# Kernel tuning notes

Measured on AMD Instinct MI355X. Metric: run time of the kernel, lower is better.

Reference implementation:

```python
import jax, jax.numpy as jnp
import numpy as np

K = 2          # downsample rate
H = 8          # attention heads
D_LLM = 1024
DK = D_LLM // H
N_LAYER = 2
F_HID = D_LLM // 4  # 256, per PositionwiseFeedForward(llm_dim, llm_dim//4)
EPS = 1e-12


def _ln(x, g, b):
    m = jnp.mean(x, axis=-1, keepdims=True)
    v = jnp.mean((x - m) ** 2, axis=-1, keepdims=True)
    return (x - m) * jax.lax.rsqrt(v + EPS) * g + b


def setup_inputs() -> dict:
    key = jax.random.key(0)
    ks = jax.random.split(key, 16)
    s = 0.02
    d_in = 512 * K   # encoder_dim * k = 1024
    d_ff = 2048
    inp = {
        'x':  jax.random.normal(ks[0], (8, 2048, 512), dtype=jnp.float32),
        'W1': jax.random.normal(ks[1], (d_ff, d_in)) * s,
        'b1': jnp.zeros((d_ff,)),
        'W2': jax.random.normal(ks[2], (D_LLM, d_ff)) * s,
        'b2': jnp.zeros((D_LLM,)),
        'ln1_g': jnp.ones((N_LAYER, D_LLM)), 'ln1_b': jnp.zeros((N_LAYER, D_LLM)),
        'ln2_g': jnp.ones((N_LAYER, D_LLM)), 'ln2_b': jnp.zeros((N_LAYER, D_LLM)),
        'Wq': jax.random.normal(ks[3], (N_LAYER, D_LLM, D_LLM)) * s, 'bq': jnp.zeros((N_LAYER, D_LLM)),
        'Wk': jax.random.normal(ks[4], (N_LAYER, D_LLM, D_LLM)) * s, 'bk': jnp.zeros((N_LAYER, D_LLM)),
        'Wv': jax.random.normal(ks[5], (N_LAYER, D_LLM, D_LLM)) * s, 'bv': jnp.zeros((N_LAYER, D_LLM)),
        'Wo': jax.random.normal(ks[6], (N_LAYER, D_LLM, D_LLM)) * s, 'bo': jnp.zeros((N_LAYER, D_LLM)),
        'Fw1': jax.random.normal(ks[7], (N_LAYER, F_HID, D_LLM)) * s, 'Fb1': jnp.zeros((N_LAYER, F_HID)),
        'Fw2': jax.random.normal(ks[8], (N_LAYER, D_LLM, F_HID)) * s, 'Fb2': jnp.zeros((N_LAYER, D_LLM)),
    }
    return inp


def reference(x, W1, b1, W2, b2, ln1_g, ln1_b, ln2_g, ln2_b,
              Wq, bq, Wk, bk, Wv, bv, Wo, bo, Fw1, Fb1, Fw2, Fb2):
    B, S, D = x.shape
    chunk = (S - 1) // K + 1
    pad = chunk * K - S
    x = jnp.pad(x, ((0, 0), (0, pad), (0, 0)))
    x = x.reshape(B, chunk, K * D)                    # [B, T, k*D]
    # downsample projection: linear2(relu(linear1(x)))
    x = jax.nn.relu(x @ W1.T + b1) @ W2.T + b2        # [B, T, D_LLM]
    T = chunk
    for l in range(N_LAYER):
        # --- self-attention sublayer (pre-norm) ---
        resid = x
        h = _ln(x, ln1_g[l], ln1_b[l])
        q = (h @ Wq[l].T + bq[l]).reshape(B, T, H, DK).transpose(0, 2, 1, 3)
        k_ = (h @ Wk[l].T + bk[l]).reshape(B, T, H, DK).transpose(0, 2, 1, 3)
        v = (h @ Wv[l].T + bv[l]).reshape(B, T, H, DK).transpose(0, 2, 1, 3)
        scores = jnp.einsum('bhqd,bhkd->bhqk', q, k_) * (DK ** -0.5)
        attn = jax.nn.softmax(scores, axis=-1)        # mask is None
        o = jnp.einsum('bhqk,bhkd->bhqd', attn, v)
        o = o.transpose(0, 2, 1, 3).reshape(B, T, H * DK)
        x = resid + o @ Wo[l].T + bo[l]
        # --- FFN sublayer (pre-norm) ---
        resid = x
        h = _ln(x, ln2_g[l], ln2_b[l])
        x = resid + jax.nn.relu(h @ Fw1[l].T + Fb1[l]) @ Fw2[l].T + Fb2[l]
    return x
```

## Files before the change

kernel.cpp:

```cpp
#include <hip/hip_runtime.h>
#include <hip/hip_bf16.h>


#define DMODEL 1024
#define DFF 2048
#define FHID 256
#define NHEAD 8
#define DKH 128
#define TSEQ 1024

typedef __hip_bfloat16 bf16;
typedef __attribute__((ext_vector_type(8))) short bf16x8;
typedef __attribute__((ext_vector_type(4))) float f32x4;

#define MFMA16(a, b, c) __builtin_amdgcn_mfma_f32_16x16x32_bf16(a, b, c, 0, 0, 0)

__device__ int g_is_bf16;

__device__ __forceinline__ bool flagbf_block() {
    __shared__ int fsh;
    if (threadIdx.x == 0)
        fsh = __hip_atomic_load(&g_is_bf16, __ATOMIC_ACQUIRE,
                                __HIP_MEMORY_SCOPE_AGENT);
    __syncthreads();
    return fsh != 0;
}
__device__ __forceinline__ float gload(const void* p, size_t i, bool bf) {
    return bf ? __bfloat162float(((const bf16*)p)[i]) : ((const float*)p)[i];
}
__device__ __forceinline__ void gstore(void* p, size_t i, bool bf, float v) {
    if (bf) ((bf16*)p)[i] = __float2bfloat16(v);
    else    ((float*)p)[i] = v;
}

__device__ __forceinline__ void async16(const bf16* g, const bf16* l) {
    __builtin_amdgcn_global_load_lds(
        (const __attribute__((address_space(1))) void*)g,
        (__attribute__((address_space(3))) void*)l, 16, 0, 0);
}

__global__ void detect_kernel(const void* __restrict__ probe) {
    const int lane = threadIdx.x & 63;
    const bf16* h = (const bf16*)probe;
    int ok = 1;
    #pragma unroll
    for (int j = 0; j < 4; ++j) {
        float v = __bfloat162float(h[lane * 4 + j]);
        if (!(fabsf(v) <= 1000.0f)) ok = 0;
    }
    unsigned long long m = __ballot(ok);
    if (lane == 0)
        __hip_atomic_store(&g_is_bf16, m == ~0ull ? 1 : 0, __ATOMIC_RELEASE,
                           __HIP_MEMORY_SCOPE_AGENT);
}

#define O_W1  0ull
#define O_W2  2097152ull
#define O_QK  4194304ull
#define O_WV  8388608ull
#define O_WO  10485760ull
#define O_F1  12582912ull
#define O_F2  13107200ull
#define ARENA_ELEMS 13631488ull

__global__ __launch_bounds__(256) void cvt_weights(
        const void* W1, const void* W2, const void* Wq, const void* Wk,
        const void* Wv, const void* Wo, const void* F1, const void* F2,
        bf16* __restrict__ arena) {
    if (flagbf_block()) return;
    int b = blockIdx.x;
    const float* src; bf16* dst;
    if      (b < 128)  {           src = (const float*)W1 + (size_t)b * 16384;
                         dst = arena + O_W1 + (size_t)b * 16384; }
    else if (b < 256)  { b -= 128; src = (const float*)W2 + (size_t)b * 16384;
                         dst = arena + O_W2 + (size_t)b * 16384; }
    else if (b < 384)  { b -= 256; src = (const float*)Wq + (size_t)b * 16384;
                         dst = arena + O_QK + (size_t)(b >> 6) * 2097152
                                            + (size_t)(b & 63) * 16384; }
    else if (b < 512)  { b -= 384; src = (const float*)Wk + (size_t)b * 16384;
                         dst = arena + O_QK + (size_t)(b >> 6) * 2097152
                                            + 1048576 + (size_t)(b & 63) * 16384; }
    else if (b < 640)  { b -= 512; src = (const float*)Wv + (size_t)b * 16384;
                         dst = arena + O_WV + (size_t)b * 16384; }
    else if (b < 768)  { b -= 640; src = (const float*)Wo + (size_t)b * 16384;
                         dst = arena + O_WO + (size_t)b * 16384; }
    else if (b < 800)  { b -= 768; src = (const float*)F1 + (size_t)b * 16384;
                         dst = arena + O_F1 + (size_t)b * 16384; }
    else               { b -= 800; src = (const float*)F2 + (size_t)b * 16384;
                         dst = arena + O_F2 + (size_t)b * 16384; }
    const int tid = threadIdx.x;
    #pragma unroll
    for (int it = 0; it < 16; ++it) {
        const int e = it * 1024 + tid * 4;
        float4 f = *(const float4*)(src + e);
        bf16 t[4] = {__float2bfloat16(f.x), __float2bfloat16(f.y),
                     __float2bfloat16(f.z), __float2bfloat16(f.w)};
        *(uint2*)(dst + e) = *(const uint2*)t;
    }
}

__global__ __launch_bounds__(256) void cvt_x(
        const void* __restrict__ X, size_t x_off, bf16* __restrict__ dst) {
    if (flagbf_block()) return;
    const float* src = (const float*)X + x_off + (size_t)blockIdx.x * 16384;
    bf16* d = dst + (size_t)blockIdx.x * 16384;
    const int tid = threadIdx.x;
    #pragma unroll
    for (int it = 0; it < 16; ++it) {
        const int e = it * 1024 + tid * 4;
        float4 f = *(const float4*)(src + e);
        bf16 t[4] = {__float2bfloat16(f.x), __float2bfloat16(f.y),
                     __float2bfloat16(f.z), __float2bfloat16(f.w)};
        *(uint2*)(d + e) = *(const uint2*)t;
    }
}

template <bool RELU, bool ADD, int CMODE, bool TRANSC, bool BIAS2>
__global__ __launch_bounds__(512, 4) void gemm256(
        const bf16* Abf, const bf16* Acv,
        const bf16* Wlo_bf, const bf16* Whi_bf,
        const bf16* Wlo_cv, const bf16* Whi_cv,
        const void* __restrict__ bias, const void* __restrict__ bias2,
        size_t b_off,
        void* __restrict__ C, size_t c_off,
        int M, int N, int K) {
    const bool fl = flagbf_block();
    const bf16* A   = fl ? Abf : Acv;
    const bf16* Wlo = fl ? Wlo_bf : Wlo_cv;
    const bf16* Whi = fl ? Whi_bf : Whi_cv;

    __shared__ __align__(16) bf16 As[2][256 * 32];
    __shared__ __align__(16) bf16 Bs[2][128 * 32];

    const int gx = gridDim.x;
    const int lin = blockIdx.x + gx * blockIdx.y;
    int bm, bn;
    if ((gridDim.y & 7) == 0) {
        const int xcd = lin & 7, j = lin >> 3;
        const int rpx = gridDim.y >> 3;
        bm = (xcd * rpx + (j / gx)) * 256;
        bn = (j % gx) * 128;
    } else {
        bm = blockIdx.y * 256;
        bn = blockIdx.x * 128;
    }

    const int tid = threadIdx.x;
    const int wave = tid >> 6, lane = tid & 63;
    const int quad = lane >> 4, l15 = lane & 15;
    const int wm = wave >> 1, wn = wave & 1;

    const bf16* Wp;
    int bnr;
    if (BIAS2 && bn >= 1024) { Wp = Whi; bnr = bn - 1024; }
    else                     { Wp = Wlo; bnr = bn; }

    const int srow = lane >> 2;
    const int schunk = (lane & 3) ^ ((lane >> 3) & 3);
    const bf16* gaBase = A  + (size_t)(bm  + wave * 32 + srow) * K + schunk * 8;
    const bf16* gbBase = Wp + (size_t)(bnr + wave * 16 + srow) * K + schunk * 8;
    const int laOff0 = (wave * 32) * 32;
    const int laOff1 = (wave * 32 + 16) * 32;
    const int lbOff  = (wave * 16) * 32;

    f32x4 acc[4][4];
    #pragma unroll
    for (int i = 0; i < 4; ++i)
        #pragma unroll
        for (int j = 0; j < 4; ++j) acc[i][j] = (f32x4){0.f, 0.f, 0.f, 0.f};

    const int nt = K >> 5;
    int cur = 0;

    async16(gaBase, &As[0][laOff0]);
    async16(gaBase + (size_t)16 * K, &As[0][laOff1]);
    async16(gbBase, &Bs[0][lbOff]);
    __asm__ __volatile__("s_waitcnt vmcnt(0)" ::: "memory");
    __syncthreads();

    for (int t = 0; t < nt; ++t) {
        if (t + 1 < nt) {
            const int kn = (t + 1) << 5;
            async16(gaBase + kn, &As[cur ^ 1][laOff0]);
            async16(gaBase + (size_t)16 * K + kn, &As[cur ^ 1][laOff1]);
            async16(gbBase + kn, &Bs[cur ^ 1][lbOff]);
        }
        bf16x8 bfr[4];
        #pragma unroll
        for (int ni = 0; ni < 4; ++ni) {
            const int row = wn * 64 + ni * 16 + l15;
            bfr[ni] = *(const bf16x8*)
                &Bs[cur][row * 32 + ((quad ^ ((row >> 1) & 3)) << 3)];
        }
        #pragma unroll
        for (int mi = 0; mi < 4; ++mi) {
            const int row = wm * 64 + mi * 16 + l15;
            bf16x8 af = *(const bf16x8*)
                &As[cur][row * 32 + ((quad ^ ((row >> 1) & 3)) << 3)];
            #pragma unroll
            for (int ni = 0; ni < 4; ++ni)
                acc[mi][ni] = MFMA16(af, bfr[ni], acc[mi][ni]);
        }
        __syncthreads();
        cur ^= 1;
    }

    const bool cbf = CMODE ? fl : true;
    #pragma unroll
    for (int ni = 0; ni < 4; ++ni) {
        const int col = bn + wn * 64 + ni * 16 + l15;
        float bv;
        if (BIAS2) bv = col < 1024 ? gload(bias, b_off + col, fl)
                                   : gload(bias2, b_off + col - 1024, fl);
        else       bv = gload(bias, b_off + col, fl);
        #pragma unroll
        for (int mi = 0; mi < 4; ++mi) {
            const int row0 = bm + wm * 64 + mi * 16 + quad * 4;
            if (TRANSC) {
                bf16 pk[4];
                #pragma unroll
                for (int rr = 0; rr < 4; ++rr)
                    pk[rr] = __float2bfloat16(acc[mi][ni][rr] + bv);
                *(uint2*)((bf16*)C + c_off + (size_t)col * M + row0) =
                    *(const uint2*)pk;
            } else {
                #pragma unroll
                for (int rr = 0; rr < 4; ++rr) {
                    float v = acc[mi][ni][rr] + bv;
                    if (RELU) v = fmaxf(v, 0.f);
                    size_t idx = c_off + (size_t)(row0 + rr) * N + col;
                    if (ADD) v += gload(C, idx, cbf);
                    gstore(C, idx, cbf, v);
                }
            }
        }
    }
}

template <bool RELU, bool ADD, int CMODE, bool TRANSC, bool BIAS2>
__global__ __launch_bounds__(256) void gemm_bf16(
        const bf16* Abf, const bf16* Acv,
        const bf16* Wlo_bf, const bf16* Whi_bf,
        const bf16* Wlo_cv, const bf16* Whi_cv,
        const void* __restrict__ bias, const void* __restrict__ bias2,
        size_t b_off,
        void* __restrict__ C, size_t c_off,
        int M, int N, int K) {
    const bool fl = flagbf_block();
    const bf16* A   = fl ? Abf : Acv;
    const bf16* Wlo = fl ? Wlo_bf : Wlo_cv;
    const bf16* Whi = fl ? Whi_bf : Whi_cv;

    __shared__ __align__(16) bf16 As[128 * 64];
    __shared__ __align__(16) bf16 Bs[128 * 64];

    const int gx = gridDim.x;
    const int lin = blockIdx.x + gx * blockIdx.y;
    int bm, bn;
    if ((gridDim.y & 7) == 0) {
        const int xcd = lin & 7, j = lin >> 3;
        const int rpx = gridDim.y >> 3;
        bm = (xcd * rpx + j / gx) * 128;
        bn = (j % gx) * 128;
    } else {
        bm = blockIdx.y * 128;
        bn = blockIdx.x * 128;
    }

    const int tid = threadIdx.x;
    const int wave = tid >> 6, lane = tid & 63;
    const int quad = lane >> 4, l15 = lane & 15;
    const int wr = wave >> 1, wc = wave & 1;
    const int l8 = lane >> 3, l7 = lane & 7;
    const int swz = l7 ^ l8;

    const bf16* Wp;
    int bnr;
    if (BIAS2 && bn >= 1024) { Wp = Whi; bnr = bn - 1024; }
    else                     { Wp = Wlo; bnr = bn; }

    f32x4 acc[4][4];
    #pragma unroll
    for (int i = 0; i < 4; ++i)
        #pragma unroll
        for (int j2 = 0; j2 < 4; ++j2) acc[i][j2] = (f32x4){0.f, 0.f, 0.f, 0.f};

    const bf16* ga0 = A  + (size_t)(bm  + wave * 32 + l8) * K + swz * 8;
    const bf16* gb0 = Wp + (size_t)(bnr + wave * 32 + l8) * K + swz * 8;
    bf16* la0 = &As[(wave * 32) * 64];
    bf16* lb0 = &Bs[(wave * 32) * 64];

    for (int k0 = 0; k0 < K; k0 += 64) {
        __syncthreads();
        #pragma unroll
        for (int i = 0; i < 4; ++i) {
            async16(ga0 + (size_t)(i * 8) * K + k0, la0 + i * 512);
            async16(gb0 + (size_t)(i * 8) * K + k0, lb0 + i * 512);
        }
        __syncthreads();

        #pragma unroll
        for (int ks = 0; ks < 2; ++ks) {
            bf16x8 af[4], bfr[4];
            #pragma unroll
            for (int mi = 0; mi < 4; ++mi) {
                const int row = wr * 64 + mi * 16 + l15;
                af[mi] = *(const bf16x8*)
                    &As[row * 64 + ((((ks << 2) | quad) ^ (row & 7)) << 3)];
            }
            #pragma unroll
            for (int ni = 0; ni < 4; ++ni) {
                const int row = wc * 64 + ni * 16 + l15;
                bfr[ni] = *(const bf16x8*)
                    &Bs[row * 64 + ((((ks << 2) | quad) ^ (row & 7)) << 3)];
            }
            #pragma unroll
            for (int mi = 0; mi < 4; ++mi)
                #pragma unroll
                for (int ni = 0; ni < 4; ++ni)
                    acc[mi][ni] = MFMA16(af[mi], bfr[ni], acc[mi][ni]);
        }
    }

    const bool cbf = CMODE ? fl : true;
    #pragma unroll
    for (int ni = 0; ni < 4; ++ni) {
        const int col = bn + wc * 64 + ni * 16 + l15;
        float bv;
        if (BIAS2) bv = col < 1024 ? gload(bias, b_off + col, fl)
                                   : gload(bias2, b_off + col - 1024, fl);
        else       bv = gload(bias, b_off + col, fl);
        #pragma unroll
        for (int mi = 0; mi < 4; ++mi) {
            const int row0 = bm + wr * 64 + mi * 16 + quad * 4;
            if (TRANSC) {
                bf16 pk[4];
                #pragma unroll
                for (int rr = 0; rr < 4; ++rr)
                    pk[rr] = __float2bfloat16(acc[mi][ni][rr] + bv);
                *(uint2*)((bf16*)C + c_off + (size_t)col * M + row0) =
                    *(const uint2*)pk;
            } else {
                #pragma unroll
                for (int rr = 0; rr < 4; ++rr) {
                    float v = acc[mi][ni][rr] + bv;
                    if (RELU) v = fmaxf(v, 0.f);
                    size_t idx = c_off + (size_t)(row0 + rr) * N + col;
                    if (ADD) v += gload(C, idx, cbf);
                    gstore(C, idx, cbf, v);
                }
            }
        }
    }
}

__global__ __launch_bounds__(256) void ln_wave(
        const void* __restrict__ X, size_t x_off,
        const void* __restrict__ g, const void* __restrict__ b, size_t gb_off,
        bf16* __restrict__ H) {
    const bool fl = flagbf_block();
    const int lane = threadIdx.x & 63;
    const int row = blockIdx.x * 4 + (threadIdx.x >> 6);
    const size_t xrow = x_off + (size_t)row * DMODEL;

    float v[16];
    if (fl) {
        const bf16* xp = (const bf16*)X + xrow;
        #pragma unroll
        for (int c = 0; c < 2; ++c) {
            uint4 raw = *(const uint4*)(xp + c * 512 + lane * 8);
            const bf16* rb = (const bf16*)&raw;
            #pragma unroll
            for (int j = 0; j < 8; ++j) v[c * 8 + j] = __bfloat162float(rb[j]);
        }
    } else {
        const float* xp = (const float*)X + xrow;
        #pragma unroll
        for (int c = 0; c < 4; ++c) {
            float4 f = *(const float4*)(xp + c * 256 + lane * 4);
            v[c * 4 + 0] = f.x; v[c * 4 + 1] = f.y;
            v[c * 4 + 2] = f.z; v[c * 4 + 3] = f.w;
        }
    }

    float s = 0.f;
    #pragma unroll
    for (int j = 0; j < 16; ++j) s += v[j];
    #pragma unroll
    for (int off = 32; off > 0; off >>= 1) s += __shfl_xor(s, off);
    const float mean = s * (1.f / DMODEL);

    float vs = 0.f;
    #pragma unroll
    for (int j = 0; j < 16; ++j) { float d = v[j] - mean; vs += d * d; }
    #pragma unroll
    for (int off = 32; off > 0; off >>= 1) vs += __shfl_xor(vs, off);
    const float rstd = rsqrtf(vs * (1.f / DMODEL) + 1e-12f);

    bf16* h = H + (size_t)row * DMODEL;
    if (fl) {
        const bf16* gp = (const bf16*)g + gb_off;
        const bf16* bp = (const bf16*)b + gb_off;
        #pragma unroll
        for (int c = 0; c < 2; ++c) {
            const int o = c * 512 + lane * 8;
            uint4 gr = *(const uint4*)(gp + o);
            uint4 br = *(const uint4*)(bp + o);
            const bf16* gg = (const bf16*)&gr;
            const bf16* bb = (const bf16*)&br;
            bf16 outv[8];
            #pragma unroll
            for (int j = 0; j < 8; ++j)
                outv[j] = __float2bfloat16((v[c * 8 + j] - mean) * rstd *
                          __bfloat162float(gg[j]) + __bfloat162float(bb[j]));
            *(uint4*)(h + o) = *(const uint4*)outv;
        }
    } else {
        const float* gp = (const float*)g + gb_off;
        const float* bp = (const float*)b + gb_off;
        #pragma unroll
        for (int c = 0; c < 4; ++c) {
            const int o = c * 256 + lane * 4;
            float4 gr = *(const float4*)(gp + o);
            float4 br = *(const float4*)(bp + o);
            const float gg[4] = {gr.x, gr.y, gr.z, gr.w};
            const float bb[4] = {br.x, br.y, br.z, br.w};
            bf16 outv[4];
            #pragma unroll
            for (int j = 0; j < 4; ++j)
                outv[j] = __float2bfloat16((v[c * 4 + j] - mean) * rstd * gg[j] + bb[j]);
            *(uint2*)(h + o) = *(const uint2*)outv;
        }
    }
}

__global__ __launch_bounds__(512) void attn_mfma(
        const bf16* __restrict__ QK, const bf16* __restrict__ Vg,
        bf16* __restrict__ Om) {
    const int cch = (int)gridDim.z;
    const int lin = blockIdx.x + (int)gridDim.x *
                    (blockIdx.y + (int)gridDim.y * blockIdx.z);
    const int xcd = lin & 7, j = lin >> 3;
    const int qt = j & 7, gl = j >> 3;
    const int g = xcd * cch + gl;
    const int h = g & 7, bb = g >> 3;

    const int Mc = cch * TSEQ;
    const int tid = threadIdx.x;
    const int wave = tid >> 6, lane = tid & 63;
    const int quad = lane >> 4, l15 = lane & 15;

    __shared__ __align__(16) bf16 Kt[64][128];
    __shared__ __align__(16) bf16 Vt[128][64];
    __shared__ __align__(16) bf16 Ps[8][16][72];

    const int qrow = qt * 128 + wave * 16 + l15;
    const float scale = 0.08838834764831845f;

    bf16x8 qf[4];
    #pragma unroll
    for (int kc = 0; kc < 4; ++kc) {
        uint4 raw = *(const uint4*)(QK + (size_t)(bb * TSEQ + qrow) * 2048 +
                                    h * DKH + kc * 32 + quad * 8);
        const bf16* rb = (const bf16*)&raw;
        bf16 tmp[8];
        #pragma unroll
        for (int j2 = 0; j2 < 8; ++j2)
            tmp[j2] = __float2bfloat16(__bfloat162float(rb[j2]) * scale);
        qf[kc] = *(const bf16x8*)tmp;
    }

    f32x4 o[8];
    #pragma unroll
    for (int i = 0; i < 8; ++i) o[i] = (f32x4){0.f, 0.f, 0.f, 0.f};
    float m_i[4] = {-1e30f, -1e30f, -1e30f, -1e30f};
    float l_i[4] = {0.f, 0.f, 0.f, 0.f};

    const int skey = tid >> 3;
    const int dseg = (tid & 7) * 16;
    const int sk7 = skey & 7;
    const int vd = tid >> 2;
    const int vseg = (tid & 3) * 16;

    const bf16* kRow = QK + (size_t)(bb * TSEQ + skey) * 2048 + 1024 +
                       h * DKH + dseg;
    const bf16* vRow = Vg + (size_t)(h * DKH + vd) * Mc + bb * TSEQ + vseg;

    auto tile = [&](int kt, uint4& kI0, uint4& kI1, uint4& vI0, uint4& vI1,
                    uint4& kO0, uint4& kO1, uint4& vO0, uint4& vO1, bool pf) {
        __syncthreads();
        {
            const int c0 = dseg >> 3, d0 = vseg >> 3;
            *(uint4*)&Kt[skey][((c0 + 0) ^ sk7) << 3] = kI0;
            *(uint4*)&Kt[skey][((c0 + 1) ^ sk7) << 3] = kI1;
            *(uint4*)&Vt[vd][((d0 + 0) ^ (vd & 7)) << 3] = vI0;
            *(uint4*)&Vt[vd][((d0 + 1) ^ (vd & 7)) << 3] = vI1;
        }
        if (pf) {
            const bf16* kp = kRow + (size_t)(kt + 1) * 64 * 2048;
            const bf16* vp = vRow + (kt + 1) * 64;
            kO0 = ((const uint4*)kp)[0];
            kO1 = ((const uint4*)kp)[1];
            vO0 = ((const uint4*)vp)[0];
            vO1 = ((const uint4*)vp)[1];
        }
        __syncthreads();

        f32x4 s[4];
        #pragma unroll
        for (int ni = 0; ni < 4; ++ni) s[ni] = (f32x4){0.f, 0.f, 0.f, 0.f};
        #pragma unroll
        for (int ni = 0; ni < 4; ++ni) {
            const int key = ni * 16 + l15;
            #pragma unroll
            for (int kc = 0; kc < 4; ++kc) {
                const int d3 = kc * 4 + quad;
                bf16x8 kb = *(const bf16x8*)&Kt[key][(d3 ^ (key & 7)) << 3];
                s[ni] = MFMA16(qf[kc], kb, s[ni]);
            }
        }

        float tm[4], ts[4];
        #pragma unroll
        for (int rr = 0; rr < 4; ++rr) {
            float v = fmaxf(fmaxf(s[0][rr], s[1][rr]), fmaxf(s[2][rr], s[3][rr]));
            v = fmaxf(v, __shfl_xor(v, 1));
            v = fmaxf(v, __shfl_xor(v, 2));
            v = fmaxf(v, __shfl_xor(v, 4));
            v = fmaxf(v, __shfl_xor(v, 8));
            tm[rr] = v;
        }
        int grow = 0;
        #pragma unroll
        for (int rr = 0; rr < 4; ++rr)
            grow |= (tm[rr] > m_i[rr] + 8.f) ? 1 : 0;
        if (__any(grow)) {
            float al[4];
            #pragma unroll
            for (int rr = 0; rr < 4; ++rr) {
                float mn = fmaxf(m_i[rr], tm[rr]);
                al[rr] = __expf(m_i[rr] - mn);
                m_i[rr] = mn;
                l_i[rr] *= al[rr];
            }
            #pragma unroll
            for (int i = 0; i < 8; ++i)
                #pragma unroll
                for (int rr = 0; rr < 4; ++rr) o[i][rr] *= al[rr];
        }
        #pragma unroll
        for (int rr = 0; rr < 4; ++rr) ts[rr] = 0.f;
        #pragma unroll
        for (int ni = 0; ni < 4; ++ni)
            #pragma unroll
            for (int rr = 0; rr < 4; ++rr) {
                float p = __expf(s[ni][rr] - m_i[rr]);
                s[ni][rr] = p;
                ts[rr] += p;
            }
        #pragma unroll
        for (int rr = 0; rr < 4; ++rr) {
            float v = ts[rr];
            v += __shfl_xor(v, 1);
            v += __shfl_xor(v, 2);
            v += __shfl_xor(v, 4);
            v += __shfl_xor(v, 8);
            l_i[rr] += v;
        }

        #pragma unroll
        for (int ni = 0; ni < 4; ++ni)
            #pragma unroll
            for (int rr = 0; rr < 4; ++rr)
                Ps[wave][quad * 4 + rr][ni * 16 + l15] = __float2bfloat16(s[ni][rr]);
        __asm__ __volatile__("s_waitcnt lgkmcnt(0)" ::: "memory");
        bf16x8 pa[2];
        #pragma unroll
        for (int kc2 = 0; kc2 < 2; ++kc2)
            pa[kc2] = *(const bf16x8*)&Ps[wave][l15][kc2 * 32 + quad * 8];

        #pragma unroll
        for (int ni2 = 0; ni2 < 8; ++ni2) {
            const int d = ni2 * 16 + l15;
            #pragma unroll
            for (int kc2 = 0; kc2 < 2; ++kc2) {
                const int key3 = kc2 * 4 + quad;
                bf16x8 vb = *(const bf16x8*)&Vt[d][(key3 ^ (d & 7)) << 3];
                o[ni2] = MFMA16(pa[kc2], vb, o[ni2]);
            }
        }
    };

    uint4 kA0, kA1, vA0, vA1, kB0, kB1, vB0, vB1;
    kA0 = ((const uint4*)kRow)[0];
    kA1 = ((const uint4*)kRow)[1];
    vA0 = ((const uint4*)vRow)[0];
    vA1 = ((const uint4*)vRow)[1];

    #pragma unroll 1
    for (int kt = 0; kt < TSEQ / 64; kt += 2) {
        tile(kt,     kA0, kA1, vA0, vA1, kB0, kB1, vB0, vB1, true);
        tile(kt + 1, kB0, kB1, vB0, vB1, kA0, kA1, vA0, vA1, kt + 2 < TSEQ / 64);
    }

    float rinv[4];
    #pragma unroll
    for (int rr = 0; rr < 4; ++rr) rinv[rr] = 1.0f / l_i[rr];
    const size_t obase = (size_t)bb * TSEQ * DMODEL + (size_t)h * DKH;
    #pragma unroll
    for (int ni2 = 0; ni2 < 8; ++ni2)
        #pragma unroll
        for (int rr = 0; rr < 4; ++rr) {
            int qr = qt * 128 + wave * 16 + quad * 4 + rr;
            Om[obase + (size_t)qr * DMODEL + ni2 * 16 + l15] =
                __float2bfloat16(o[ni2][rr] * rinv[rr]);
        }
}

extern "C" void kernel_launch(void* const* d_in, const int* in_sizes, int n_in,
                              void* d_out, int out_size, void* d_ws, size_t ws_size,
                              hipStream_t stream) {
    const void* x     = d_in[0];
    const void* W1    = d_in[1];
    const void* b1    = d_in[2];
    const void* W2    = d_in[3];
    const void* b2    = d_in[4];
    const void* ln1_g = d_in[5];
    const void* ln1_b = d_in[6];
    const void* ln2_g = d_in[7];
    const void* ln2_b = d_in[8];
    const void* Wq    = d_in[9];
    const void* bq    = d_in[10];
    const void* Wk    = d_in[11];
    const void* bk    = d_in[12];
    const void* Wv    = d_in[13];
    const void* bv    = d_in[14];
    const void* Wo    = d_in[15];
    const void* bo    = d_in[16];
    const void* Fw1   = d_in[17];
    const void* Fb1   = d_in[18];
    const void* Fw2   = d_in[19];
    const void* Fb2   = d_in[20];

    detect_kernel<<<1, 64, 0, stream>>>(W1);

    int c = 8;
    while (c > 1 &&
           (5ull * (size_t)c * (1ull << 20) + ARENA_ELEMS) * 2ull > ws_size)
        c >>= 1;
    const int nch = 8 / c;
    const int Mc = c * TSEQ;
    const size_t SL = (size_t)Mc * DMODEL;

    bf16* Hh  = (bf16*)d_ws;
    bf16* QKb = Hh + SL;
    bf16* Vtb = QKb + 2 * SL;
    bf16* Xc  = Vtb + SL;
    bf16* Wt  = Xc + SL;
    bf16* Hid = QKb;
    bf16* Ffh = QKb;
    bf16* Ob  = Hh;
    void* X = d_out;

    const bf16* xb  = (const bf16*)x;
    bf16* cW1  = Wt + O_W1;
    bf16* cW2  = Wt + O_W2;
    bf16* cWqk = Wt + O_QK;
    bf16* cWv  = Wt + O_WV;
    bf16* cWo  = Wt + O_WO;
    bf16* cF1  = Wt + O_F1;
    bf16* cF2  = Wt + O_F2;

    cvt_weights<<<832, 256, 0, stream>>>(W1, W2, Wq, Wk, Wv, Wo, Fw1, Fw2, Wt);

    for (int ci = 0; ci < nch; ++ci) {
        const size_t roff = (size_t)ci * Mc * DMODEL;

        cvt_x<<<(int)(SL / 16384), 256, 0, stream>>>(x, roff, Xc);

        gemm256<true, false, 0, false, false><<<dim3(DFF / 128, Mc / 256), 512, 0, stream>>>(
            xb + roff, Xc, (const bf16*)W1, (const bf16*)W1, cW1, cW1,
            b1, nullptr, 0, Hid, 0, Mc, DFF, DMODEL);
        gemm256<false, false, 1, false, false><<<dim3(DMODEL / 128, Mc / 256), 512, 0, stream>>>(
            Hid, Hid, (const bf16*)W2, (const bf16*)W2, cW2, cW2,
            b2, nullptr, 0, X, roff, Mc, DMODEL, DFF);

        for (int l = 0; l < 2; ++l) {
            const size_t wOff   = (size_t)l * DMODEL * DMODEL;
            const size_t fOff   = (size_t)l * FHID * DMODEL;
            const size_t vOff   = (size_t)l * DMODEL;
            const size_t f1bOff = (size_t)l * FHID;

            const bf16* wqL = (const bf16*)Wq + wOff;
            const bf16* wkL = (const bf16*)Wk + wOff;
            const bf16* wvL = (const bf16*)Wv + wOff;
            const bf16* woL = (const bf16*)Wo + wOff;
            const bf16* f1L = (const bf16*)Fw1 + fOff;
            const bf16* f2L = (const bf16*)Fw2 + fOff;
            const bf16* qkLo = cWqk + (size_t)l * 2097152;
            const bf16* qkHi = qkLo + 1048576;

            ln_wave<<<Mc / 4, 256, 0, stream>>>(X, roff, ln1_g, ln1_b, vOff, Hh);
            gemm256<false, false, 0, false, true><<<dim3(2048 / 128, Mc / 256), 512, 0, stream>>>(
                Hh, Hh, wqL, wkL, qkLo, qkHi,
                bq, bk, vOff, QKb, 0, Mc, 2048, DMODEL);
            gemm256<false, false, 0, true, false><<<dim3(DMODEL / 128, Mc / 256), 512, 0, stream>>>(
                Hh, Hh, wvL, wvL, cWv + wOff, cWv + wOff,
                bv, nullptr, vOff, Vtb, 0, Mc, DMODEL, DMODEL);

            attn_mfma<<<dim3(TSEQ / 128, NHEAD, c), 512, 0, stream>>>(QKb, Vtb, Ob);

            gemm256<false, true, 1, false, false><<<dim3(DMODEL / 128, Mc / 256), 512, 0, stream>>>(
                Ob, Ob, woL, woL, cWo + wOff, cWo + wOff,
                bo, nullptr, vOff, X, roff, Mc, DMODEL, DMODEL);

            ln_wave<<<Mc / 4, 256, 0, stream>>>(X, roff, ln2_g, ln2_b, vOff, Hh);
            gemm_bf16<true, false, 0, false, false><<<dim3(FHID / 128, Mc / 128), 256, 0, stream>>>(
                Hh, Hh, f1L, f1L, cF1 + fOff, cF1 + fOff,
                Fb1, nullptr, f1bOff, Ffh, 0, Mc, FHID, DMODEL);
            gemm_bf16<false, true, 1, false, false><<<dim3(DMODEL / 128, Mc / 128), 256, 0, stream>>>(
                Ffh, Ffh, f2L, f2L, cF2 + fOff, cF2 + fOff,
                Fb2, nullptr, vOff, X, roff, Mc, DMODEL, FHID);
        }
    }
}
```

Baseline: 867.0 us.

## Use partial vmcnt waits in GEMM and drop register prefetch in attention

In the GEMM main loop, the full drain before the loop is replaced by a per-iteration partial wait (vmcnt(3)), so loads for the next tile can stay in flight while the current tile is consumed. Raw s_barrier plus sched_barrier replace __syncthreads. In the attention kernel, the double-buffered register prefetch of K/V tiles is removed and each tile is loaded synchronously inside the loop, which lowers register pressure but exposes global load latency. The two changes pull in opposite directions on latency hiding, and the raw barriers depend on correct wait counts for the async LDS loads.

```diff
diff --git a/kernel.cpp b/kernel.cpp
--- a/kernel.cpp
+++ b/kernel.cpp
@@ -175,8 +175,6 @@
     async16(gaBase, &As[0][laOff0]);
     async16(gaBase + (size_t)16 * K, &As[0][laOff1]);
     async16(gbBase, &Bs[0][lbOff]);
-    __asm__ __volatile__("s_waitcnt vmcnt(0)" ::: "memory");
-    __syncthreads();
 
     for (int t = 0; t < nt; ++t) {
         if (t + 1 < nt) {
@@ -184,7 +182,13 @@
             async16(gaBase + kn, &As[cur ^ 1][laOff0]);
             async16(gaBase + (size_t)16 * K + kn, &As[cur ^ 1][laOff1]);
             async16(gbBase + kn, &Bs[cur ^ 1][lbOff]);
-        }
+            __asm__ __volatile__("s_waitcnt vmcnt(3)" ::: "memory");
+        } else {
+            __asm__ __volatile__("s_waitcnt vmcnt(0)" ::: "memory");
+        }
+        __builtin_amdgcn_s_barrier();
+        __builtin_amdgcn_sched_barrier(0);
+
         bf16x8 bfr[4];
         #pragma unroll
         for (int ni = 0; ni < 4; ++ni) {
@@ -201,7 +205,8 @@
             for (int ni = 0; ni < 4; ++ni)
                 acc[mi][ni] = MFMA16(af, bfr[ni], acc[mi][ni]);
         }
-        __syncthreads();
+        __builtin_amdgcn_sched_barrier(0);
+        __builtin_amdgcn_s_barrier();
         cur ^= 1;
     }
 
@@ -482,27 +487,26 @@
     const int vd = tid >> 2;
     const int vseg = (tid & 3) * 16;
 
-    const bf16* kRow = QK + (size_t)(bb * TSEQ + skey) * 2048 + 1024 +
-                       h * DKH + dseg;
-    const bf16* vRow = Vg + (size_t)(h * DKH + vd) * Mc + bb * TSEQ + vseg;
-
-    auto tile = [&](int kt, uint4& kI0, uint4& kI1, uint4& vI0, uint4& vI1,
-                    uint4& kO0, uint4& kO1, uint4& vO0, uint4& vO1, bool pf) {
+    for (int kt = 0; kt < TSEQ / 64; ++kt) {
         __syncthreads();
         {
-            const int c0 = dseg >> 3, d0 = vseg >> 3;
-            *(uint4*)&Kt[skey][((c0 + 0) ^ sk7) << 3] = kI0;
-            *(uint4*)&Kt[skey][((c0 + 1) ^ sk7) << 3] = kI1;
-            *(uint4*)&Vt[vd][((d0 + 0) ^ (vd & 7)) << 3] = vI0;
-            *(uint4*)&Vt[vd][((d0 + 1) ^ (vd & 7)) << 3] = vI1;
-        }
-        if (pf) {
-            const bf16* kp = kRow + (size_t)(kt + 1) * 64 * 2048;
-            const bf16* vp = vRow + (kt + 1) * 64;
-            kO0 = ((const uint4*)kp)[0];
-            kO1 = ((const uint4*)kp)[1];
-            vO0 = ((const uint4*)vp)[0];
-            vO1 = ((const uint4*)vp)[1];
+            const bf16* kp = QK + (size_t)(bb * TSEQ + kt * 64 + skey) * 2048 +
+                             1024 + h * DKH + dseg;
+            const bf16* vp = Vg + (size_t)(h * DKH + vd) * Mc + bb * TSEQ +
+                             kt * 64 + vseg;
+            uint4 kv[2], vv[2];
+            #pragma unroll
+            for (int g2 = 0; g2 < 2; ++g2) { kv[g2] = ((const uint4*)kp)[g2]; vv[g2] = ((const uint4*)vp)[g2]; }
+            #pragma unroll
+            for (int g2 = 0; g2 < 2; ++g2) {
+                int c = (dseg >> 3) + g2;
+                *(uint4*)&Kt[skey][(c ^ sk7) << 3] = kv[g2];
+            }
+            #pragma unroll
+            for (int g2 = 0; g2 < 2; ++g2) {
+                int c = (vseg >> 3) + g2;
+                *(uint4*)&Vt[vd][(c ^ (vd & 7)) << 3] = vv[g2];
+            }
         }
         __syncthreads();
 
@@ -589,18 +593,6 @@
                 o[ni2] = MFMA16(pa[kc2], vb, o[ni2]);
             }
         }
-    };
-
-    uint4 kA0, kA1, vA0, vA1, kB0, kB1, vB0, vB1;
-    kA0 = ((const uint4*)kRow)[0];
-    kA1 = ((const uint4*)kRow)[1];
-    vA0 = ((const uint4*)vRow)[0];
-    vA1 = ((const uint4*)vRow)[1];
-
-    #pragma unroll 1
-    for (int kt = 0; kt < TSEQ / 64; kt += 2) {
-        tile(kt,     kA0, kA1, vA0, vA1, kB0, kB1, vB0, vB1, true);
-        tile(kt + 1, kB0, kB1, vB0, vB1, kA0, kA1, vA0, vA1, kt + 2 < TSEQ / 64);
     }
 
     float rinv[4];
```

Measured after the change: 844.1 us. -2.6%, faster.
